# Optimization experiments

Hardware: AMD Instinct MI355X
Metric: run time of the kernel (lower is better)

## Reference

```python
import jax, jax.numpy as jnp
import numpy as np

B, H, O, D = 1024, 256, 128, 64
LN_EPS = 1e-6  # flax LayerNorm default


def _layer_norm(h, scale, bias):
    mu = jnp.mean(h, axis=-1, keepdims=True)
    var = jnp.mean((h - mu) ** 2, axis=-1, keepdims=True)
    return (h - mu) * jax.lax.rsqrt(var + LN_EPS) * scale + bias


def _readout(hm, ln_scale, ln_bias, Wout, bout):
    return _layer_norm(hm, ln_scale, ln_bias) @ Wout + bout


def setup_inputs() -> dict:
    key = jax.random.key(0)
    ks = jax.random.split(key, 16)
    n = jax.random.normal
    s_i = 1.0 / np.sqrt(D)
    s_h = 1.0 / np.sqrt(H)
    return {
        # forward args (batched over B independent sequences)
        "x": n(ks[0], (B, D)),
        "y": n(ks[1], (B, O)),
        "m": jnp.ones((B, O), jnp.float32),
        "h": n(ks[2], (B, H)) * 0.1,
        "delta": n(ks[3], (B, H)) * 0.1,
        "inst_delta": n(ks[4], (B, H)) * 0.1,
        "prod_jac": n(ks[5], (B, H, H)) * 0.05,
        "prev_mean": n(ks[6], (B, H)) * 0.1,
        "t": jnp.zeros((B,), jnp.float32),
        # GRU params (flax Dense kernels are [in, out])
        "Wiz": n(ks[7], (D, H)) * s_i, "biz": jnp.zeros((H,)),
        "Whz": n(ks[8], (H, H)) * s_h,
        "Wir": n(ks[9], (D, H)) * s_i, "bir": jnp.zeros((H,)),
        "Whr": n(ks[10], (H, H)) * s_h,
        "Win": n(ks[11], (D, H)) * s_i, "bin_": jnp.zeros((H,)),
        "Whn": n(ks[12], (H, H)) * s_h, "bhn": jnp.zeros((H,)),
        # readout params
        "ln_scale": jnp.ones((H,)), "ln_bias": jnp.zeros((H,)),
        "Wout": n(ks[13], (H, O)) * s_h, "bout": jnp.zeros((O,)),
    }


def reference(x, y, m, h, delta, inst_delta, prod_jac, prev_mean, t,
              Wiz, biz, Whz, Wir, bir, Whr, Win, bin_, Whn, bhn,
              ln_scale, ln_bias, Wout, bout):
    # --- GRU recurrence ---
    r = jax.nn.sigmoid(x @ Wir + bir + h @ Whr)
    z = jax.nn.sigmoid(x @ Wiz + biz + h @ Whz)
    g = h @ Whn + bhn
    n_ = jnp.tanh(x @ Win + bin_ + r * g)
    new_h = (1.0 - z) * n_ + z * h

    new_t = t + 1.0
    new_mean = new_h  # pooling == 'none'
    out = _readout(new_mean, ln_scale, ln_bias, Wout, bout)

    # --- analytic d new_h / d h  (== jax.jacfwd(recurrence, 0)) ---
    dz = z * (1.0 - z)
    dr = r * (1.0 - r)
    dn = 1.0 - n_ * n_
    # J[b,i,j] = d new_h_i / d h_j
    J = (((h - n_) * dz)[:, :, None] * Whz.T
         + ((1.0 - z) * dn * r)[:, :, None] * Whn.T
         + ((1.0 - z) * dn * g * dr)[:, :, None] * Whr.T
         + z[:, :, None] * jnp.eye(H, dtype=z.dtype))
    jac = jnp.swapaxes(J, -1, -2)  # module transposes the jacfwd output

    new_prod_jac = jnp.einsum('bij,bjk->bik', prod_jac, jac)
    # exact inverse path (approx_inverse=False)
    new_delta = jnp.einsum('bij,bj->bi', jnp.linalg.inv(jac), delta - inst_delta)

    # inst_delta = grad of masked-MSE loss wrt new_mean through the readout
    ro = lambda hm: _readout(hm, ln_scale, ln_bias, Wout, bout)
    o2, vjp = jax.vjp(ro, new_mean)
    g_o = 2.0 * m * (o2 - y)  # dL/do for L = sum(m*(o-y)^2)
    (new_inst_delta,) = vjp(g_o)

    delta_output = 2.0 * m * (out - y)
    h_norm = jnp.linalg.norm(new_h, axis=-1)
    delta_norm = jnp.linalg.norm(new_delta, axis=-1)
    prod_jac_norm = jnp.sqrt(jnp.sum(new_prod_jac ** 2, axis=(-2, -1)))

    return (new_h, new_delta, new_inst_delta, new_prod_jac, new_mean, new_t,
            out, h, delta_output, h_norm, delta_norm, prod_jac_norm, jac)
```

## Files before the change

kernel.cpp:

```cpp
#include <hip/hip_runtime.h>
#include <hip/hip_bf16.h>

#define B_N 1024
#define H_N 256
#define O_N 128
#define D_N 64

#define OFF_NEWH      0
#define OFF_NEWDELTA  262144
#define OFF_NEWINST   524288
#define OFF_NEWPJ     786432
#define OFF_NEWMEAN   67895296
#define OFF_NEWT      68157440
#define OFF_OUT       68158464
#define OFF_HCOPY     68289536
#define OFF_DELTAOUT  68551680
#define OFF_HNORM     68682752
#define OFF_DNORM     68683776
#define OFF_PJNORM    68684800
#define OFF_JAC       68685824

typedef __attribute__((ext_vector_type(8))) short short8;
typedef __attribute__((ext_vector_type(4))) float f32x4;

__device__ __forceinline__ short f2bf(float f){
  union { float f; unsigned u; } v; v.f = f;
  unsigned r = v.u + 0x7fffu + ((v.u >> 16) & 1u);
  return (short)(r >> 16);
}

__device__ __forceinline__ float wave_reduce_sum(float v){
  #pragma unroll
  for (int off = 32; off > 0; off >>= 1) v += __shfl_xor(v, off);
  return v;
}

__global__ __launch_bounds__(256) void gates_kernel(
    const float* __restrict__ x, const float* __restrict__ h, const float* __restrict__ tt,
    const float* __restrict__ Wiz, const float* __restrict__ biz, const float* __restrict__ Whz,
    const float* __restrict__ Wir, const float* __restrict__ bir, const float* __restrict__ Whr,
    const float* __restrict__ Win, const float* __restrict__ bin_, const float* __restrict__ Whn,
    const float* __restrict__ bhn,
    float* __restrict__ dout, float* __restrict__ ws)
{
  int b = blockIdx.x, j = threadIdx.x;
  __shared__ float xs[64];
  __shared__ float hs[256];
  __shared__ float red[4];
  if (j < 64) xs[j] = x[b*64 + j];
  float hj = h[b*256 + j];
  hs[j] = hj;
  __syncthreads();

  float zp = biz[j], rp = bir[j], np = bin_[j], g = bhn[j];
  #pragma unroll 8
  for (int k = 0; k < 64; k++){
    float xv = xs[k];
    zp = fmaf(xv, Wiz[k*256 + j], zp);
    rp = fmaf(xv, Wir[k*256 + j], rp);
    np = fmaf(xv, Win[k*256 + j], np);
  }
  #pragma unroll 8
  for (int k = 0; k < 256; k++){
    float hv = hs[k];
    zp = fmaf(hv, Whz[k*256 + j], zp);
    rp = fmaf(hv, Whr[k*256 + j], rp);
    g  = fmaf(hv, Whn[k*256 + j], g);
  }
  float r = 1.f / (1.f + expf(-rp));
  float z = 1.f / (1.f + expf(-zp));
  float n = tanhf(np + r*g);
  float nh = (1.f - z)*n + z*hj;

  float dz = z*(1.f - z);
  float dn = 1.f - n*n;
  float drv = r*(1.f - r);
  float az = (hj - n)*dz;
  float an = (1.f - z)*dn*r;
  float ar = (1.f - z)*dn*g*drv;

  dout[OFF_NEWH   + b*256 + j] = nh;
  dout[OFF_NEWMEAN+ b*256 + j] = nh;
  dout[OFF_HCOPY  + b*256 + j] = hj;
  ws[0*262144 + b*256 + j] = z;
  ws[1*262144 + b*256 + j] = az;
  ws[2*262144 + b*256 + j] = an;
  ws[3*262144 + b*256 + j] = ar;

  float s = wave_reduce_sum(nh*nh);
  if ((j & 63) == 0) red[j >> 6] = s;
  __syncthreads();
  if (j == 0){
    dout[OFF_HNORM + b] = sqrtf(red[0] + red[1] + red[2] + red[3]);
    dout[OFF_NEWT + b] = tt[b] + 1.f;
  }
}

__global__ __launch_bounds__(1024, 4) void solve_kernel(
    const float* __restrict__ Whz, const float* __restrict__ Whn, const float* __restrict__ Whr,
    const float* __restrict__ ws, const float* __restrict__ delta,
    const float* __restrict__ inst_delta, float* __restrict__ dout)
{
  const int b = blockIdx.x, tid = threadIdx.x;
  const int l  = tid & 63;
  const int w  = tid >> 6;
  const int wr = w >> 2, wc = w & 3;
  const int lr = l >> 3, lc = l & 7;
  const int r0 = wr*64 + lr*8;
  const int c0 = wc*64 + lc*8;

  __shared__ __align__(16) float panelC[8*264];
  __shared__ __align__(16) float rowsbuf[8*264];
  __shared__ __align__(16) float rhs[256];
  __shared__ __align__(16) float pivval_s[256];
  __shared__ int   perm_s[256];

  float A[8][8];
  {
    float* jac_out = dout + OFF_JAC + (size_t)b*65536;
    #pragma unroll
    for (int half = 0; half < 2; half++){
      const int cb = c0 + half*4;
      float4 vz4 = *(const float4*)(ws + 0*262144 + b*256 + cb);
      float4 va4 = *(const float4*)(ws + 1*262144 + b*256 + cb);
      float4 vn4 = *(const float4*)(ws + 2*262144 + b*256 + cb);
      float4 vr4 = *(const float4*)(ws + 3*262144 + b*256 + cb);
      float zc[4] = {vz4.x, vz4.y, vz4.z, vz4.w};
      float az[4] = {va4.x, va4.y, va4.z, va4.w};
      float an[4] = {vn4.x, vn4.y, vn4.z, vn4.w};
      float ar[4] = {vr4.x, vr4.y, vr4.z, vr4.w};
      #pragma unroll
      for (int i = 0; i < 8; i++){
        const int row = r0 + i;
        float4 wz = *(const float4*)(Whz + row*256 + cb);
        float4 wn = *(const float4*)(Whn + row*256 + cb);
        float4 wq = *(const float4*)(Whr + row*256 + cb);
        A[i][half*4+0] = fmaf(wz.x, az[0], fmaf(wn.x, an[0], wq.x*ar[0]));
        A[i][half*4+1] = fmaf(wz.y, az[1], fmaf(wn.y, an[1], wq.y*ar[1]));
        A[i][half*4+2] = fmaf(wz.z, az[2], fmaf(wn.z, an[2], wq.z*ar[2]));
        A[i][half*4+3] = fmaf(wz.w, az[3], fmaf(wn.w, an[3], wq.w*ar[3]));
        #pragma unroll
        for (int k = 0; k < 4; k++)
          if (cb + k == row) A[i][half*4+k] += zc[k];
        *(float4*)(jac_out + row*256 + cb) =
            make_float4(A[i][half*4+0], A[i][half*4+1], A[i][half*4+2], A[i][half*4+3]);
      }
    }
  }

  if (tid < 256) rhs[tid] = delta[b*256 + tid] - inst_delta[b*256 + tid];

  unsigned usedbits = 0u;

  for (int kb = 0; kb < 32; kb++){
    if (wc == (kb >> 3) && lc == (kb & 7)){
      #pragma unroll
      for (int c = 0; c < 8; c++){
        *(float4*)&panelC[c*264 + r0]     = make_float4(A[0][c], A[1][c], A[2][c], A[3][c]);
        *(float4*)&panelC[c*264 + r0 + 4] = make_float4(A[4][c], A[5][c], A[6][c], A[7][c]);
      }
    }
    __syncthreads();

    if (w == 0){
      float4 cur = *(const float4*)&panelC[0*264 + 4*l];
      #pragma unroll
      for (int j = 0; j < 8; j++){
        float c4[4] = {cur.x, cur.y, cur.z, cur.w};
        unsigned key = 0u;
        #pragma unroll
        for (int q = 0; q < 4; q++){
          unsigned kq = (__float_as_uint(fabsf(c4[q])) & 0xFFFFFF00u) | (unsigned)(l*4 + q);
          bool fresh = ((usedbits >> q) & 1u) == 0u;
          key = (fresh && kq > key) ? kq : key;
        }
        #pragma unroll
        for (int off = 32; off > 0; off >>= 1){
          unsigned ok = __shfl_xor(key, off);
          key = ok > key ? ok : key;
        }
        const int p = (int)(key & 255u);
        float sel = c4[0];
        #pragma unroll
        for (int q = 1; q < 4; q++) sel = ((p & 3) == q) ? c4[q] : sel;
        const float pv = __shfl(sel, p >> 2);
        const float ipv = 1.0f / pv;
        if ((p >> 2) == l) usedbits |= 1u << (p & 3);
        const bool own = ((p >> 2) == l);
        float d4[4];
        #pragma unroll
        for (int q = 0; q < 4; q++){
          float dv = c4[q] * ipv;
          d4[q] = (own && (p & 3) == q) ? 0.f : dv;
        }
        float prow[8];
        #pragma unroll
        for (int c = 0; c < 8; c++) prow[c] = panelC[c*264 + p];
        #pragma unroll
        for (int c = 0; c < 8; c++){
          if (c == j){
            *(float4*)&panelC[j*264 + 4*l] = make_float4(d4[0], d4[1], d4[2], d4[3]);
          } else {
            float4 pc = *(const float4*)&panelC[c*264 + 4*l];
            pc.x = fmaf(-d4[0], prow[c], pc.x);
            pc.y = fmaf(-d4[1], prow[c], pc.y);
            pc.z = fmaf(-d4[2], prow[c], pc.z);
            pc.w = fmaf(-d4[3], prow[c], pc.w);
            if (c == j + 1) cur = pc;
            else *(float4*)&panelC[c*264 + 4*l] = pc;
          }
        }
        if (l == 0){ perm_s[kb*8 + j] = p; pivval_s[kb*8 + j] = pv; }
      }
    }
    __syncthreads();

    {
      int pq[8];
      #pragma unroll
      for (int q = 0; q < 8; q++) pq[q] = perm_s[kb*8 + q];
      #pragma unroll
      for (int i = 0; i < 8; i++){
        int qm = -1;
        #pragma unroll
        for (int q = 0; q < 8; q++) qm = (pq[q] == r0 + i) ? q : qm;
        if (qm >= 0){
          *(float4*)&rowsbuf[qm*264 + c0]     = make_float4(A[i][0], A[i][1], A[i][2], A[i][3]);
          *(float4*)&rowsbuf[qm*264 + c0 + 4] = make_float4(A[i][4], A[i][5], A[i][6], A[i][7]);
        }
      }
    }
    float rhsP[8];
    if (tid < 256){
      #pragma unroll
      for (int q = 0; q < 8; q++) rhsP[q] = rhs[perm_s[kb*8 + q]];
    }
    __syncthreads();

    #pragma unroll 1
    for (int q = 0; q < 8; q++){
      float4 d0 = *(const float4*)&panelC[q*264 + r0];
      float4 d1 = *(const float4*)&panelC[q*264 + r0 + 4];
      float4 ra = *(const float4*)&rowsbuf[q*264 + c0];
      float4 rb = *(const float4*)&rowsbuf[q*264 + c0 + 4];
      float dq[8] = {d0.x, d0.y, d0.z, d0.w, d1.x, d1.y, d1.z, d1.w};
      float rq[8] = {ra.x, ra.y, ra.z, ra.w, rb.x, rb.y, rb.z, rb.w};
      #pragma unroll
      for (int i = 0; i < 8; i++)
        #pragma unroll
        for (int j = 0; j < 8; j++)
          A[i][j] = fmaf(-dq[i], rq[j], A[i][j]);
    }
    if (tid < 256){
      float rv = rhs[tid];
      #pragma unroll 1
      for (int q = 0; q < 8; q++) rv = fmaf(-panelC[q*264 + tid], rhsP[q], rv);
      rhs[tid] = rv;
    }
    __syncthreads();
  }

  if (tid < 256){
    float xv = rhs[perm_s[tid]] / pivval_s[tid];
    dout[OFF_NEWDELTA + b*256 + tid] = xv;
    rowsbuf[tid] = xv*xv;
  }
  __syncthreads();
  if (tid < 64){
    float s = rowsbuf[tid] + rowsbuf[tid+64] + rowsbuf[tid+128] + rowsbuf[tid+192];
    s = wave_reduce_sum(s);
    if (tid == 0) dout[OFF_DNORM + b] = sqrtf(s);
  }
}

__global__ __launch_bounds__(512) void pj_gemm_kernel(
    const float* __restrict__ prod_jac, const float* __restrict__ jac,
    float* __restrict__ out_pj, float* __restrict__ out_norm)
{
  int b = blockIdx.x, tid = threadIdx.x;
  int l = tid & 63, wid = tid >> 6;
  int wm = wid >> 2, wn = wid & 3;
  int lr = l & 15, lg = l >> 4;

  __shared__ float As[256*33];
  __shared__ float Bs[256*33];

  const float* Ag = prod_jac + (size_t)b*65536;
  const float* Bg = jac      + (size_t)b*65536;

  f32x4 acc[8][4];
  #pragma unroll
  for (int i = 0; i < 8; i++)
    #pragma unroll
    for (int jn = 0; jn < 4; jn++) acc[i][jn] = (f32x4){0.f,0.f,0.f,0.f};

  const int arow = tid >> 1, acolb = (tid & 1)*16;
  const int bk = tid >> 4, bcolb = (tid & 15)*16;

  for (int kt = 0; kt < 8; ++kt){
    const int k0 = kt*32;
    __syncthreads();
    {
      const float4* asrc = (const float4*)(Ag + arow*256 + k0 + acolb);
      float* ad = &As[arow*33 + acolb];
      #pragma unroll
      for (int q = 0; q < 4; q++){
        float4 v = asrc[q];
        ad[q*4+0]=v.x; ad[q*4+1]=v.y; ad[q*4+2]=v.z; ad[q*4+3]=v.w;
      }
      const float4* bsrc = (const float4*)(Bg + (k0 + bk)*256 + bcolb);
      #pragma unroll
      for (int q = 0; q < 4; q++){
        float4 v = bsrc[q];
        Bs[(bcolb+q*4+0)*33 + bk] = v.x;
        Bs[(bcolb+q*4+1)*33 + bk] = v.y;
        Bs[(bcolb+q*4+2)*33 + bk] = v.z;
        Bs[(bcolb+q*4+3)*33 + bk] = v.w;
      }
    }
    __syncthreads();

    short8 bfr[4];
    #pragma unroll
    for (int ni = 0; ni < 4; ni++){
      const float* bp = &Bs[(wn*64 + ni*16 + lr)*33 + lg*8];
      short8 t;
      #pragma unroll
      for (int v = 0; v < 8; v++) t[v] = f2bf(bp[v]);
      bfr[ni] = t;
    }
    #pragma unroll
    for (int mi = 0; mi < 8; mi++){
      const float* ap = &As[(wm*128 + mi*16 + lr)*33 + lg*8];
      short8 af;
      #pragma unroll
      for (int v = 0; v < 8; v++) af[v] = f2bf(ap[v]);
      #pragma unroll
      for (int ni = 0; ni < 4; ni++)
        acc[mi][ni] = __builtin_amdgcn_mfma_f32_16x16x32_bf16(af, bfr[ni], acc[mi][ni], 0, 0, 0);
    }
  }

  float nrm = 0.f;
  #pragma unroll
  for (int mi = 0; mi < 8; mi++){
    #pragma unroll
    for (int ni = 0; ni < 4; ni++){
      #pragma unroll
      for (int rr = 0; rr < 4; rr++){
        int row = wm*128 + mi*16 + lg*4 + rr;
        int col = wn*64 + ni*16 + lr;
        float vv = acc[mi][ni][rr];
        out_pj[(size_t)b*65536 + row*256 + col] = vv;
        nrm += vv*vv;
      }
    }
  }
  __syncthreads();
  As[tid] = nrm;
  __syncthreads();
  if (tid < 64){
    float s = 0.f;
    #pragma unroll
    for (int q = 0; q < 8; q++) s += As[tid + q*64];
    s = wave_reduce_sum(s);
    if (tid == 0) out_norm[b] = sqrtf(s);
  }
}

__global__ __launch_bounds__(256) void readout_kernel(
    const float* __restrict__ y, const float* __restrict__ m,
    const float* __restrict__ ln_scale, const float* __restrict__ ln_bias,
    const float* __restrict__ Wout, const float* __restrict__ bout,
    float* __restrict__ dout)
{
  int b = blockIdx.x, j = threadIdx.x;
  __shared__ float lno[256], xh[256], go[128], red2[256], red[4];

  float hv = dout[OFF_NEWH + b*256 + j];
  float s = wave_reduce_sum(hv);
  if ((j & 63) == 0) red[j >> 6] = s;
  __syncthreads();
  float mu = (red[0] + red[1] + red[2] + red[3]) * (1.f/256.f);
  __syncthreads();
  float d = hv - mu;
  float sv = wave_reduce_sum(d*d);
  if ((j & 63) == 0) red[j >> 6] = sv;
  __syncthreads();
  float var = (red[0] + red[1] + red[2] + red[3]) * (1.f/256.f);
  float rstd = rsqrtf(var + 1e-6f);
  float xhj = d * rstd;
  xh[j] = xhj;
  lno[j] = xhj * ln_scale[j] + ln_bias[j];
  __syncthreads();

  int i = j & 127, half = j >> 7;
  float part = half ? 0.f : bout[i];
  #pragma unroll 8
  for (int jj = half*128; jj < half*128 + 128; jj++)
    part = fmaf(lno[jj], Wout[jj*128 + i], part);
  red2[j] = part;
  __syncthreads();
  if (j < 128){
    float o = red2[j] + red2[j + 128];
    float gv = 2.f * m[b*128 + j] * (o - y[b*128 + j]);
    dout[OFF_OUT + b*128 + j] = o;
    dout[OFF_DELTAOUT + b*128 + j] = gv;
    go[j] = gv;
  }
  __syncthreads();

  float gl = 0.f;
  const float4* wrow = (const float4*)(Wout + j*128);
  #pragma unroll 8
  for (int q = 0; q < 32; q++){
    float4 w = wrow[q];
    gl = fmaf(w.x, go[q*4+0], gl);
    gl = fmaf(w.y, go[q*4+1], gl);
    gl = fmaf(w.z, go[q*4+2], gl);
    gl = fmaf(w.w, go[q*4+3], gl);
  }
  float gx = gl * ln_scale[j];
  __syncthreads();
  float t1 = wave_reduce_sum(gx);
  if ((j & 63) == 0) red[j >> 6] = t1;
  __syncthreads();
  float s1 = (red[0] + red[1] + red[2] + red[3]) * (1.f/256.f);
  __syncthreads();
  float t2 = wave_reduce_sum(gx * xhj);
  if ((j & 63) == 0) red[j >> 6] = t2;
  __syncthreads();
  float s2m = (red[0] + red[1] + red[2] + red[3]) * (1.f/256.f);
  float nid = rstd * (gx - s1 - xhj * s2m);
  dout[OFF_NEWINST + b*256 + j] = nid;
}

extern "C" void kernel_launch(void* const* d_in, const int* in_sizes, int n_in,
                              void* d_out, int out_size, void* d_ws, size_t ws_size,
                              hipStream_t stream) {
  const float* x          = (const float*)d_in[0];
  const float* y          = (const float*)d_in[1];
  const float* m          = (const float*)d_in[2];
  const float* h          = (const float*)d_in[3];
  const float* delta      = (const float*)d_in[4];
  const float* inst_delta = (const float*)d_in[5];
  const float* prod_jac   = (const float*)d_in[6];
  const float* t          = (const float*)d_in[8];
  const float* Wiz  = (const float*)d_in[9];
  const float* biz  = (const float*)d_in[10];
  const float* Whz  = (const float*)d_in[11];
  const float* Wir  = (const float*)d_in[12];
  const float* bir  = (const float*)d_in[13];
  const float* Whr  = (const float*)d_in[14];
  const float* Win  = (const float*)d_in[15];
  const float* bin_ = (const float*)d_in[16];
  const float* Whn  = (const float*)d_in[17];
  const float* bhn  = (const float*)d_in[18];
  const float* ln_scale = (const float*)d_in[19];
  const float* ln_bias  = (const float*)d_in[20];
  const float* Wout = (const float*)d_in[21];
  const float* bout = (const float*)d_in[22];

  float* dout = (float*)d_out;
  float* ws = (float*)d_ws;

  gates_kernel<<<1024, 256, 0, stream>>>(x, h, t, Wiz, biz, Whz, Wir, bir, Whr,
                                         Win, bin_, Whn, bhn, dout, ws);
  solve_kernel<<<1024, 1024, 0, stream>>>(Whz, Whn, Whr, ws, delta, inst_delta, dout);
  pj_gemm_kernel<<<1024, 512, 0, stream>>>(prod_jac, dout + OFF_JAC,
                                           dout + OFF_NEWPJ, dout + OFF_PJNORM);
  readout_kernel<<<1024, 256, 0, stream>>>(y, m, ln_scale, ln_bias, Wout, bout, dout);
}
```

Before: 1.710 ms.

## Add lookahead to blocked LU solve, overlapping panel factorization with trailing update

Double-buffers the panel storage so that wave 0 factors the next 8-column panel while the other waves apply the previous panel's rank-8 update to their register tiles. The thread owning the next panel updates it early, right after the row exchange, and writes it into the alternate buffer. The right-hand-side update moves to threads 256-511 so it does not compete with wave 0. The goal is to take the serial pivot search and panel elimination off the critical path, at the cost of extra shared memory and a more complex synchronization scheme.

```diff
diff --git a/kernel.cpp b/kernel.cpp
--- a/kernel.cpp
+++ b/kernel.cpp
@@ -109,8 +109,8 @@
   const int r0 = wr*64 + lr*8;
   const int c0 = wc*64 + lc*8;
 
-  __shared__ __align__(16) float panelC[8*264];
-  __shared__ __align__(16) float rowsbuf[8*264];
+  __shared__ __align__(16) float PC[2][8*264];
+  __shared__ __align__(16) float RB[8*264];
   __shared__ __align__(16) float rhs[256];
   __shared__ __align__(16) float pivval_s[256];
   __shared__ int   perm_s[256];
@@ -150,23 +150,27 @@
 
   if (tid < 256) rhs[tid] = delta[b*256 + tid] - inst_delta[b*256 + tid];
 
+  if (wc == 0 && lc == 0){
+    #pragma unroll
+    for (int c = 0; c < 8; c++){
+      *(float4*)&PC[0][c*264 + r0]     = make_float4(A[0][c], A[1][c], A[2][c], A[3][c]);
+      *(float4*)&PC[0][c*264 + r0 + 4] = make_float4(A[4][c], A[5][c], A[6][c], A[7][c]);
+    }
+  }
   unsigned usedbits = 0u;
+  float rhsP[8];
+  __syncthreads();
 
   for (int kb = 0; kb < 32; kb++){
-    if (wc == (kb >> 3) && lc == (kb & 7)){
-      #pragma unroll
-      for (int c = 0; c < 8; c++){
-        *(float4*)&panelC[c*264 + r0]     = make_float4(A[0][c], A[1][c], A[2][c], A[3][c]);
-        *(float4*)&panelC[c*264 + r0 + 4] = make_float4(A[4][c], A[5][c], A[6][c], A[7][c]);
-      }
-    }
-    __syncthreads();
+    const int cur = kb & 1;
+    float* __restrict__ Dc = &PC[cur][0];
+    float* __restrict__ Dp = &PC[cur ^ 1][0];
 
     if (w == 0){
-      float4 cur = *(const float4*)&panelC[0*264 + 4*l];
+      float4 curc = *(const float4*)&Dc[0*264 + 4*l];
       #pragma unroll
       for (int j = 0; j < 8; j++){
-        float c4[4] = {cur.x, cur.y, cur.z, cur.w};
+        float c4[4] = {curc.x, curc.y, curc.z, curc.w};
         unsigned key = 0u;
         #pragma unroll
         for (int q = 0; q < 4; q++){
@@ -195,22 +199,48 @@
         }
         float prow[8];
         #pragma unroll
-        for (int c = 0; c < 8; c++) prow[c] = panelC[c*264 + p];
+        for (int c = 0; c < 8; c++) prow[c] = Dc[c*264 + p];
         #pragma unroll
         for (int c = 0; c < 8; c++){
           if (c == j){
-            *(float4*)&panelC[j*264 + 4*l] = make_float4(d4[0], d4[1], d4[2], d4[3]);
+            *(float4*)&Dc[j*264 + 4*l] = make_float4(d4[0], d4[1], d4[2], d4[3]);
           } else {
-            float4 pc = *(const float4*)&panelC[c*264 + 4*l];
+            float4 pc = *(const float4*)&Dc[c*264 + 4*l];
             pc.x = fmaf(-d4[0], prow[c], pc.x);
             pc.y = fmaf(-d4[1], prow[c], pc.y);
             pc.z = fmaf(-d4[2], prow[c], pc.z);
             pc.w = fmaf(-d4[3], prow[c], pc.w);
-            if (c == j + 1) cur = pc;
-            else *(float4*)&panelC[c*264 + 4*l] = pc;
+            if (c == j + 1) curc = pc;
+            else *(float4*)&Dc[c*264 + 4*l] = pc;
           }
         }
         if (l == 0){ perm_s[kb*8 + j] = p; pivval_s[kb*8 + j] = pv; }
+      }
+    }
+    if (kb > 0){
+      const bool early = (wc == (kb >> 3)) && (lc == (kb & 7));
+      if (!early){
+        #pragma unroll 1
+        for (int q = 0; q < 8; q++){
+          float4 d0 = *(const float4*)&Dp[q*264 + r0];
+          float4 d1 = *(const float4*)&Dp[q*264 + r0 + 4];
+          float4 ra = *(const float4*)&RB[q*264 + c0];
+          float4 rb4 = *(const float4*)&RB[q*264 + c0 + 4];
+          float dq[8] = {d0.x, d0.y, d0.z, d0.w, d1.x, d1.y, d1.z, d1.w};
+          float rq[8] = {ra.x, ra.y, ra.z, ra.w, rb4.x, rb4.y, rb4.z, rb4.w};
+          #pragma unroll
+          for (int i = 0; i < 8; i++)
+            #pragma unroll
+            for (int j = 0; j < 8; j++)
+              A[i][j] = fmaf(-dq[i], rq[j], A[i][j]);
+        }
+      }
+      if (tid >= 256 && tid < 512){
+        const int e = tid - 256;
+        float rv = rhs[e];
+        #pragma unroll 1
+        for (int q = 0; q < 8; q++) rv = fmaf(-Dp[q*264 + e], rhsP[q], rv);
+        rhs[e] = rv;
       }
     }
     __syncthreads();
@@ -225,49 +255,61 @@
         #pragma unroll
         for (int q = 0; q < 8; q++) qm = (pq[q] == r0 + i) ? q : qm;
         if (qm >= 0){
-          *(float4*)&rowsbuf[qm*264 + c0]     = make_float4(A[i][0], A[i][1], A[i][2], A[i][3]);
-          *(float4*)&rowsbuf[qm*264 + c0 + 4] = make_float4(A[i][4], A[i][5], A[i][6], A[i][7]);
-        }
-      }
-    }
-    float rhsP[8];
-    if (tid < 256){
-      #pragma unroll
-      for (int q = 0; q < 8; q++) rhsP[q] = rhs[perm_s[kb*8 + q]];
+          *(float4*)&RB[qm*264 + c0]     = make_float4(A[i][0], A[i][1], A[i][2], A[i][3]);
+          *(float4*)&RB[qm*264 + c0 + 4] = make_float4(A[i][4], A[i][5], A[i][6], A[i][7]);
+        }
+      }
+      if (tid >= 256 && tid < 512){
+        #pragma unroll
+        for (int q = 0; q < 8; q++) rhsP[q] = rhs[pq[q]];
+      }
     }
     __syncthreads();
 
+    if (kb < 31){
+      const bool owner = (wc == ((kb+1) >> 3)) && (lc == ((kb+1) & 7));
+      if (owner){
+        #pragma unroll 1
+        for (int q = 0; q < 8; q++){
+          float4 d0 = *(const float4*)&Dc[q*264 + r0];
+          float4 d1 = *(const float4*)&Dc[q*264 + r0 + 4];
+          float4 ra = *(const float4*)&RB[q*264 + c0];
+          float4 rb4 = *(const float4*)&RB[q*264 + c0 + 4];
+          float dq[8] = {d0.x, d0.y, d0.z, d0.w, d1.x, d1.y, d1.z, d1.w};
+          float rq[8] = {ra.x, ra.y, ra.z, ra.w, rb4.x, rb4.y, rb4.z, rb4.w};
+          #pragma unroll
+          for (int i = 0; i < 8; i++)
+            #pragma unroll
+            for (int j = 0; j < 8; j++)
+              A[i][j] = fmaf(-dq[i], rq[j], A[i][j]);
+        }
+        #pragma unroll
+        for (int c = 0; c < 8; c++){
+          *(float4*)&Dp[c*264 + r0]     = make_float4(A[0][c], A[1][c], A[2][c], A[3][c]);
+          *(float4*)&Dp[c*264 + r0 + 4] = make_float4(A[4][c], A[5][c], A[6][c], A[7][c]);
+        }
+      }
+    }
+    __syncthreads();
+  }
+
+  if (tid >= 256 && tid < 512){
+    const int e = tid - 256;
+    float rv = rhs[e];
     #pragma unroll 1
-    for (int q = 0; q < 8; q++){
-      float4 d0 = *(const float4*)&panelC[q*264 + r0];
-      float4 d1 = *(const float4*)&panelC[q*264 + r0 + 4];
-      float4 ra = *(const float4*)&rowsbuf[q*264 + c0];
-      float4 rb = *(const float4*)&rowsbuf[q*264 + c0 + 4];
-      float dq[8] = {d0.x, d0.y, d0.z, d0.w, d1.x, d1.y, d1.z, d1.w};
-      float rq[8] = {ra.x, ra.y, ra.z, ra.w, rb.x, rb.y, rb.z, rb.w};
-      #pragma unroll
-      for (int i = 0; i < 8; i++)
-        #pragma unroll
-        for (int j = 0; j < 8; j++)
-          A[i][j] = fmaf(-dq[i], rq[j], A[i][j]);
-    }
-    if (tid < 256){
-      float rv = rhs[tid];
-      #pragma unroll 1
-      for (int q = 0; q < 8; q++) rv = fmaf(-panelC[q*264 + tid], rhsP[q], rv);
-      rhs[tid] = rv;
-    }
-    __syncthreads();
-  }
+    for (int q = 0; q < 8; q++) rv = fmaf(-PC[1][q*264 + e], rhsP[q], rv);
+    rhs[e] = rv;
+  }
+  __syncthreads();
 
   if (tid < 256){
     float xv = rhs[perm_s[tid]] / pivval_s[tid];
     dout[OFF_NEWDELTA + b*256 + tid] = xv;
-    rowsbuf[tid] = xv*xv;
+    RB[tid] = xv*xv;
   }
   __syncthreads();
   if (tid < 64){
-    float s = rowsbuf[tid] + rowsbuf[tid+64] + rowsbuf[tid+128] + rowsbuf[tid+192];
+    float s = RB[tid] + RB[tid+64] + RB[tid+128] + RB[tid+192];
     s = wave_reduce_sum(s);
     if (tid == 0) dout[OFF_DNORM + b] = sqrtf(s);
   }
```

Result: slower. 1.908 ms (+11.6%).

## Register-resident panel factorization and fold next-panel write into trailing update

Applied to the files above, without the earlier changes.

The pivot wave now keeps the 8-column panel in registers, fetches pivot rows with shuffles instead of LDS reads, and writes the factored panel into a separate Dt buffer. The next panel is written to panelC at the end of the trailing update, which removes one __syncthreads per block step, and the trailing-update loop software-prefetches the next rank-1 operands. The trailing update is skipped on the last step. This targets barrier and LDS latency on the serial LU critical path, at the cost of extra shared memory and register pressure under a 1024-thread launch bound.

```diff
diff --git a/kernel.cpp b/kernel.cpp
--- a/kernel.cpp
+++ b/kernel.cpp
@@ -110,7 +110,8 @@
   const int c0 = wc*64 + lc*8;
 
   __shared__ __align__(16) float panelC[8*264];
-  __shared__ __align__(16) float rowsbuf[8*264];
+  __shared__ __align__(16) float Dt[8*264];
+  __shared__ __align__(16) float RB[8*264];
   __shared__ __align__(16) float rhs[256];
   __shared__ __align__(16) float pivval_s[256];
   __shared__ int   perm_s[256];
@@ -150,23 +151,24 @@
 
   if (tid < 256) rhs[tid] = delta[b*256 + tid] - inst_delta[b*256 + tid];
 
+  if (wc == 0 && lc == 0){
+    #pragma unroll
+    for (int c = 0; c < 8; c++){
+      *(float4*)&panelC[c*264 + r0]     = make_float4(A[0][c], A[1][c], A[2][c], A[3][c]);
+      *(float4*)&panelC[c*264 + r0 + 4] = make_float4(A[4][c], A[5][c], A[6][c], A[7][c]);
+    }
+  }
   unsigned usedbits = 0u;
+  __syncthreads();
 
   for (int kb = 0; kb < 32; kb++){
-    if (wc == (kb >> 3) && lc == (kb & 7)){
-      #pragma unroll
-      for (int c = 0; c < 8; c++){
-        *(float4*)&panelC[c*264 + r0]     = make_float4(A[0][c], A[1][c], A[2][c], A[3][c]);
-        *(float4*)&panelC[c*264 + r0 + 4] = make_float4(A[4][c], A[5][c], A[6][c], A[7][c]);
-      }
-    }
-    __syncthreads();
-
     if (w == 0){
-      float4 cur = *(const float4*)&panelC[0*264 + 4*l];
+      float4 P[8];
+      #pragma unroll
+      for (int c = 0; c < 8; c++) P[c] = *(const float4*)&panelC[c*264 + 4*l];
       #pragma unroll
       for (int j = 0; j < 8; j++){
-        float c4[4] = {cur.x, cur.y, cur.z, cur.w};
+        float c4[4] = {P[j].x, P[j].y, P[j].z, P[j].w};
         unsigned key = 0u;
         #pragma unroll
         for (int q = 0; q < 4; q++){
@@ -180,81 +182,100 @@
           key = ok > key ? ok : key;
         }
         const int p = (int)(key & 255u);
+        const int psl = p >> 2, pq = p & 3;
         float sel = c4[0];
         #pragma unroll
-        for (int q = 1; q < 4; q++) sel = ((p & 3) == q) ? c4[q] : sel;
-        const float pv = __shfl(sel, p >> 2);
+        for (int q = 1; q < 4; q++) sel = (pq == q) ? c4[q] : sel;
+        const float pv = __shfl(sel, psl);
         const float ipv = 1.0f / pv;
-        if ((p >> 2) == l) usedbits |= 1u << (p & 3);
-        const bool own = ((p >> 2) == l);
+        if (psl == l) usedbits |= 1u << pq;
+        float prow[8];
+        #pragma unroll
+        for (int c = 0; c < 8; c++){
+          float s = P[c].x;
+          s = (pq == 1) ? P[c].y : s;
+          s = (pq == 2) ? P[c].z : s;
+          s = (pq == 3) ? P[c].w : s;
+          prow[c] = __shfl(s, psl);
+        }
+        const bool own = (psl == l);
         float d4[4];
         #pragma unroll
         for (int q = 0; q < 4; q++){
           float dv = c4[q] * ipv;
-          d4[q] = (own && (p & 3) == q) ? 0.f : dv;
-        }
-        float prow[8];
-        #pragma unroll
-        for (int c = 0; c < 8; c++) prow[c] = panelC[c*264 + p];
+          d4[q] = (own && pq == q) ? 0.f : dv;
+        }
         #pragma unroll
         for (int c = 0; c < 8; c++){
-          if (c == j){
-            *(float4*)&panelC[j*264 + 4*l] = make_float4(d4[0], d4[1], d4[2], d4[3]);
-          } else {
-            float4 pc = *(const float4*)&panelC[c*264 + 4*l];
-            pc.x = fmaf(-d4[0], prow[c], pc.x);
-            pc.y = fmaf(-d4[1], prow[c], pc.y);
-            pc.z = fmaf(-d4[2], prow[c], pc.z);
-            pc.w = fmaf(-d4[3], prow[c], pc.w);
-            if (c == j + 1) cur = pc;
-            else *(float4*)&panelC[c*264 + 4*l] = pc;
-          }
-        }
+          if (c == j) continue;
+          P[c].x = fmaf(-d4[0], prow[c], P[c].x);
+          P[c].y = fmaf(-d4[1], prow[c], P[c].y);
+          P[c].z = fmaf(-d4[2], prow[c], P[c].z);
+          P[c].w = fmaf(-d4[3], prow[c], P[c].w);
+        }
+        P[j] = make_float4(d4[0], d4[1], d4[2], d4[3]);
         if (l == 0){ perm_s[kb*8 + j] = p; pivval_s[kb*8 + j] = pv; }
       }
+      #pragma unroll
+      for (int c = 0; c < 8; c++) *(float4*)&Dt[c*264 + 4*l] = P[c];
     }
     __syncthreads();
 
-    {
-      int pq[8];
-      #pragma unroll
-      for (int q = 0; q < 8; q++) pq[q] = perm_s[kb*8 + q];
-      #pragma unroll
-      for (int i = 0; i < 8; i++){
-        int qm = -1;
-        #pragma unroll
-        for (int q = 0; q < 8; q++) qm = (pq[q] == r0 + i) ? q : qm;
-        if (qm >= 0){
-          *(float4*)&rowsbuf[qm*264 + c0]     = make_float4(A[i][0], A[i][1], A[i][2], A[i][3]);
-          *(float4*)&rowsbuf[qm*264 + c0 + 4] = make_float4(A[i][4], A[i][5], A[i][6], A[i][7]);
-        }
+    int pq8[8];
+    #pragma unroll
+    for (int q = 0; q < 8; q++) pq8[q] = perm_s[kb*8 + q];
+    #pragma unroll
+    for (int i = 0; i < 8; i++){
+      int qm = -1;
+      #pragma unroll
+      for (int q = 0; q < 8; q++) qm = (pq8[q] == r0 + i) ? q : qm;
+      if (qm >= 0){
+        *(float4*)&RB[qm*264 + c0]     = make_float4(A[i][0], A[i][1], A[i][2], A[i][3]);
+        *(float4*)&RB[qm*264 + c0 + 4] = make_float4(A[i][4], A[i][5], A[i][6], A[i][7]);
       }
     }
     float rhsP[8];
     if (tid < 256){
       #pragma unroll
-      for (int q = 0; q < 8; q++) rhsP[q] = rhs[perm_s[kb*8 + q]];
+      for (int q = 0; q < 8; q++) rhsP[q] = rhs[pq8[q]];
     }
     __syncthreads();
 
-    #pragma unroll 1
-    for (int q = 0; q < 8; q++){
-      float4 d0 = *(const float4*)&panelC[q*264 + r0];
-      float4 d1 = *(const float4*)&panelC[q*264 + r0 + 4];
-      float4 ra = *(const float4*)&rowsbuf[q*264 + c0];
-      float4 rb = *(const float4*)&rowsbuf[q*264 + c0 + 4];
-      float dq[8] = {d0.x, d0.y, d0.z, d0.w, d1.x, d1.y, d1.z, d1.w};
-      float rq[8] = {ra.x, ra.y, ra.z, ra.w, rb.x, rb.y, rb.z, rb.w};
-      #pragma unroll
-      for (int i = 0; i < 8; i++)
-        #pragma unroll
-        for (int j = 0; j < 8; j++)
-          A[i][j] = fmaf(-dq[i], rq[j], A[i][j]);
+    if (kb < 31){
+      float4 d0 = *(const float4*)&Dt[0*264 + r0];
+      float4 d1 = *(const float4*)&Dt[0*264 + r0 + 4];
+      float4 ra = *(const float4*)&RB[0*264 + c0];
+      float4 rb4 = *(const float4*)&RB[0*264 + c0 + 4];
+      #pragma unroll 1
+      for (int q = 0; q < 8; q++){
+        float4 nd0, nd1, nra, nrb;
+        if (q < 7){
+          nd0 = *(const float4*)&Dt[(q+1)*264 + r0];
+          nd1 = *(const float4*)&Dt[(q+1)*264 + r0 + 4];
+          nra = *(const float4*)&RB[(q+1)*264 + c0];
+          nrb = *(const float4*)&RB[(q+1)*264 + c0 + 4];
+        }
+        float dq[8] = {d0.x, d0.y, d0.z, d0.w, d1.x, d1.y, d1.z, d1.w};
+        float rq[8] = {ra.x, ra.y, ra.z, ra.w, rb4.x, rb4.y, rb4.z, rb4.w};
+        #pragma unroll
+        for (int i = 0; i < 8; i++)
+          #pragma unroll
+          for (int j = 0; j < 8; j++)
+            A[i][j] = fmaf(-dq[i], rq[j], A[i][j]);
+        d0 = nd0; d1 = nd1; ra = nra; rb4 = nrb;
+      }
+      if (wc == ((kb+1) >> 3) && lc == ((kb+1) & 7)){
+        #pragma unroll
+        for (int c = 0; c < 8; c++){
+          *(float4*)&panelC[c*264 + r0]     = make_float4(A[0][c], A[1][c], A[2][c], A[3][c]);
+          *(float4*)&panelC[c*264 + r0 + 4] = make_float4(A[4][c], A[5][c], A[6][c], A[7][c]);
+        }
+      }
     }
     if (tid < 256){
       float rv = rhs[tid];
       #pragma unroll 1
-      for (int q = 0; q < 8; q++) rv = fmaf(-panelC[q*264 + tid], rhsP[q], rv);
+      for (int q = 0; q < 8; q++) rv = fmaf(-Dt[q*264 + tid], rhsP[q], rv);
       rhs[tid] = rv;
     }
     __syncthreads();
@@ -263,11 +284,11 @@
   if (tid < 256){
     float xv = rhs[perm_s[tid]] / pivval_s[tid];
     dout[OFF_NEWDELTA + b*256 + tid] = xv;
-    rowsbuf[tid] = xv*xv;
+    RB[tid] = xv*xv;
   }
   __syncthreads();
   if (tid < 64){
-    float s = rowsbuf[tid] + rowsbuf[tid+64] + rowsbuf[tid+128] + rowsbuf[tid+192];
+    float s = RB[tid] + RB[tid+64] + RB[tid+128] + RB[tid+192];
     s = wave_reduce_sum(s);
     if (tid == 0) dout[OFF_DNORM + b] = sqrtf(s);
   }
```

Measured after the change: 5.329 ms. 212% more time.
